# Kernel tuning notes

Hardware: AMD Instinct MI355X
Metric: run time of the kernel (lower is better)

Reference implementation:

```python
import jax, jax.numpy as jnp
import numpy as np

H = 1024      # hidden_size
E = 8         # num_experts
I = 1024      # moe_intermediate_size
SI = 2816     # shared_expert_intermediate_size
B, S = 2, 2048


def setup_inputs() -> dict:
    key = jax.random.key(0)
    ks = jax.random.split(key, 10)
    sc = lambda fan_in: 1.0 / np.sqrt(fan_in)
    return {
        "hidden_states": jax.random.normal(ks[0], (B, S, H), dtype=jnp.float32),
        "gate_w": jax.random.normal(ks[1], (E, H), dtype=jnp.float32) * sc(H),
        "wg": jax.random.normal(ks[2], (E, I, H), dtype=jnp.float32) * sc(H),   # gate_proj per expert
        "wu": jax.random.normal(ks[3], (E, I, H), dtype=jnp.float32) * sc(H),   # up_proj per expert
        "wd": jax.random.normal(ks[4], (E, H, I), dtype=jnp.float32) * sc(I),   # down_proj per expert
        "swg": jax.random.normal(ks[5], (SI, H), dtype=jnp.float32) * sc(H),    # shared gate_proj
        "swu": jax.random.normal(ks[6], (SI, H), dtype=jnp.float32) * sc(H),    # shared up_proj
        "swd": jax.random.normal(ks[7], (H, SI), dtype=jnp.float32) * sc(SI),   # shared down_proj
        "shared_gate_w": jax.random.normal(ks[8], (1, H), dtype=jnp.float32) * sc(H),
        "top_k": 2,
    }


def reference(hidden_states, gate_w, wg, wu, wd, swg, swu, swd, shared_gate_w, top_k):
    b, s, h = hidden_states.shape
    flat = hidden_states.reshape(-1, h)                      # [T,H]
    # router
    logits = flat @ gate_w.T                                 # [T,E]
    probs = jax.nn.softmax(logits, axis=-1)
    vals, idx = jax.lax.top_k(probs, top_k)                  # [T,K]
    vals = vals / jnp.sum(vals, axis=-1, keepdims=True)      # norm_topk_prob
    # combine weights scattered to full expert dim: [T,E]
    combine = jnp.sum(jax.nn.one_hot(idx, E, dtype=flat.dtype) * vals[..., None], axis=1)
    # dense per-expert SwiGLU FFN over all tokens, masked-combined (same math)
    g = jax.nn.silu(jnp.einsum("th,eih->eti", flat, wg))     # [E,T,I]
    u = jnp.einsum("th,eih->eti", flat, wu)
    eo = jnp.einsum("eti,ehi->eth", g * u, wd)               # [E,T,H]
    expert_out = jnp.einsum("te,eth->th", combine, eo)       # [T,H]
    # shared expert with sigmoid gate
    shared = (jax.nn.silu(flat @ swg.T) * (flat @ swu.T)) @ swd.T   # [T,H]
    sgate = jax.nn.sigmoid(flat @ shared_gate_w.T)           # [T,1]
    out = expert_out + sgate * shared
    return out.reshape(b, s, h)
```

## Files before the change

kernel.cpp:

```cpp
#include <hip/hip_runtime.h>
#include <stdint.h>

#define TT  4096
#define HD  1024
#define NE  8
#define ID  1024
#define SID 2816

typedef short s16x8 __attribute__((ext_vector_type(8)));
typedef float f32x4 __attribute__((ext_vector_type(4)));
typedef float f32x4v __attribute__((ext_vector_type(4)));
typedef unsigned short u16x4 __attribute__((ext_vector_type(4)));

__device__ __forceinline__ ushort f2bf(float f) {
  uint32_t u = __float_as_uint(f);
  u += 0x7FFFu + ((u >> 16) & 1u);
  return (ushort)(u >> 16);
}

__device__ __forceinline__ float bf2f(ushort u) {
  return __uint_as_float((uint32_t)u << 16);
}

__device__ __forceinline__ void gll16(const ushort* g, ushort* l) {
  __builtin_amdgcn_global_load_lds(
      (const __attribute__((address_space(1))) void*)g,
      (__attribute__((address_space(3))) void*)l, 16, 0, 0);
}

struct CvtArgs {
  const float* src[7];
  ushort* dst[7];
  int n[7];
};

__global__ __launch_bounds__(256) void cvt_all(CvtArgs a) {
  int t = blockIdx.y;
  int i = (blockIdx.x * 256 + threadIdx.x) * 4;
  if (i >= a.n[t]) return;
  f32x4v v = *(const f32x4v*)(a.src[t] + i);
  u16x4 o;
  o.x = f2bf(v.x); o.y = f2bf(v.y); o.z = f2bf(v.z); o.w = f2bf(v.w);
  *(u16x4*)(a.dst[t] + i) = o;
}

__global__ __launch_bounds__(256) void router_k(
    const float* __restrict__ X, const float* __restrict__ gw,
    const float* __restrict__ sgw,
    int* __restrict__ topki, float* __restrict__ topkw,
    float* __restrict__ sgate) {
  __shared__ float gwL[(NE + 1) * HD];
  #pragma unroll
  for (int i = 0; i < NE * HD / 1024; i++) {
    int idx = i * 1024 + threadIdx.x * 4;
    *(f32x4*)&gwL[idx] = *(const f32x4*)&gw[idx];
  }
  {
    int idx = threadIdx.x * 4;
    if (idx < HD) *(f32x4*)&gwL[NE * HD + idx] = *(const f32x4*)&sgw[idx];
  }
  __syncthreads();

  const int wave = threadIdx.x >> 6, lane = threadIdx.x & 63;
  #pragma unroll
  for (int tt = 0; tt < 4; tt++) {
    const int t = blockIdx.x * 16 + wave * 4 + tt;
    const float* x = X + (size_t)t * HD;
    float acc[NE + 1];
    #pragma unroll
    for (int e = 0; e <= NE; e++) acc[e] = 0.f;
    #pragma unroll
    for (int p = 0; p < HD / 256; p++) {
      const int k = p * 256 + lane * 4;
      f32x4 xv = *(const f32x4*)&x[k];
      #pragma unroll
      for (int e = 0; e < NE; e++) {
        f32x4 g = *(const f32x4*)&gwL[e * HD + k];
        acc[e] += xv.x * g.x + xv.y * g.y + xv.z * g.z + xv.w * g.w;
      }
      f32x4 s = *(const f32x4*)&gwL[NE * HD + k];
      acc[NE] += xv.x * s.x + xv.y * s.y + xv.z * s.z + xv.w * s.w;
    }
    #pragma unroll
    for (int off = 32; off > 0; off >>= 1)
      #pragma unroll
      for (int e = 0; e <= NE; e++)
        acc[e] += __shfl_xor(acc[e], off, 64);
    if (lane == 0) {
      float m = acc[0];
      #pragma unroll
      for (int e = 1; e < NE; e++) m = fmaxf(m, acc[e]);
      float p[NE];
      #pragma unroll
      for (int e = 0; e < NE; e++) p[e] = __expf(acc[e] - m);
      int i1 = 0;
      #pragma unroll
      for (int e = 1; e < NE; e++) if (p[e] > p[i1]) i1 = e;
      int i2 = (i1 == 0) ? 1 : 0;
      #pragma unroll
      for (int e = 0; e < NE; e++) if (e != i1 && p[e] > p[i2]) i2 = e;
      float inv = 1.f / (p[i1] + p[i2]);
      topki[2 * t] = i1; topki[2 * t + 1] = i2;
      topkw[2 * t] = p[i1] * inv; topkw[2 * t + 1] = p[i2] * inv;
      sgate[t] = 1.f / (1.f + __expf(-acc[NE]));
    }
  }
}

__global__ __launch_bounds__(1024) void binning_k(
    const int* __restrict__ topki, const float* __restrict__ topkw,
    int* __restrict__ cnt, int* __restrict__ offs,
    int* __restrict__ tokmap, float* __restrict__ wmap,
    int* __restrict__ smap) {
  __shared__ int h[NE];
  __shared__ int base[NE];
  const int tid = threadIdx.x;
  if (tid < NE) h[tid] = 0;
  __syncthreads();
  int my_e[8];
  #pragma unroll
  for (int i = 0; i < 8; i++) {
    int s = i * 1024 + tid;
    my_e[i] = topki[s];
    atomicAdd(&h[my_e[i]], 1);
  }
  __syncthreads();
  if (tid == 0) {
    int o = 0;
    for (int e = 0; e < NE; e++) {
      base[e] = o; offs[e] = o; cnt[e] = h[e]; o += h[e];
    }
  }
  __syncthreads();
  #pragma unroll
  for (int i = 0; i < 8; i++) {
    int s = i * 1024 + tid;
    int pos = atomicAdd(&base[my_e[i]], 1);
    tokmap[pos] = s >> 1;
    wmap[pos] = topkw[s];
    smap[s] = pos;
  }
}

constexpr int BM = 128, BN = 128, BK = 32;

template <bool GATHER>
__device__ __forceinline__ void gu_core(
    const ushort* __restrict__ A, const ushort* __restrict__ Wg,
    const ushort* __restrict__ Wu, ushort* __restrict__ Hout,
    const int* __restrict__ tokmap, int cnt, int seg,
    int mb, int nb, int N, int K) {
  const int m0 = mb * BM;
  if (m0 >= cnt) return;
  const int n0 = nb * BN;

  __shared__ ushort lA[2][BM * BK];
  __shared__ ushort lBg[2][BN * BK];
  __shared__ ushort lBu[2][BN * BK];

  const int tid = threadIdx.x;
  const int wave = tid >> 6, lane = tid & 63;
  const int wm = (wave >> 1) * 64, wn = (wave & 1) * 64;

  const int ar0 = wave * 32 + (lane >> 2);
  const int ar1 = ar0 + 16;
  const int kc = ((lane & 3) ^ ((lane >> 3) & 3)) * 8;

  const ushort *a0p, *a1p;
  if (GATHER) {
    int m_ = m0 + ar0;
    int tk0 = (m_ < cnt) ? tokmap[seg + m_] : 0;
    m_ = m0 + ar1;
    int tk1 = (m_ < cnt) ? tokmap[seg + m_] : 0;
    a0p = A + (size_t)tk0 * K + kc;
    a1p = A + (size_t)tk1 * K + kc;
  } else {
    a0p = A + (size_t)(m0 + ar0) * K + kc;
    a1p = A + (size_t)(m0 + ar1) * K + kc;
  }
  const ushort* bg0 = Wg + (size_t)(n0 + ar0) * K + kc;
  const ushort* bg1 = Wg + (size_t)(n0 + ar1) * K + kc;
  const ushort* bu0 = Wu + (size_t)(n0 + ar0) * K + kc;
  const ushort* bu1 = Wu + (size_t)(n0 + ar1) * K + kc;

  f32x4 accG[4][4], accU[4][4];
  #pragma unroll
  for (int i = 0; i < 4; i++)
    #pragma unroll
    for (int j = 0; j < 4; j++) {
      accG[i][j] = f32x4{0.f, 0.f, 0.f, 0.f};
      accU[i][j] = f32x4{0.f, 0.f, 0.f, 0.f};
    }

  const int lr = lane & 15;
  const int lk = (((lane >> 4) ^ ((lr >> 1) & 3))) * 8;
  const int w32 = wave * 32;

  auto stage = [&](int b, int k0) {
    gll16(a0p + k0, &lA[b][w32 * BK]);
    gll16(a1p + k0, &lA[b][(w32 + 16) * BK]);
    gll16(bg0 + k0, &lBg[b][w32 * BK]);
    gll16(bg1 + k0, &lBg[b][(w32 + 16) * BK]);
    gll16(bu0 + k0, &lBu[b][w32 * BK]);
    gll16(bu1 + k0, &lBu[b][(w32 + 16) * BK]);
  };

  const int nt = K / BK;
  stage(0, 0);
  for (int t = 0; t < nt; t++) {
    const int cur = t & 1;
    if (t + 1 < nt) {
      stage(cur ^ 1, (t + 1) * BK);
      asm volatile("s_waitcnt vmcnt(6)" ::: "memory");
    } else {
      asm volatile("s_waitcnt vmcnt(0)" ::: "memory");
    }
    __builtin_amdgcn_s_barrier();

    s16x8 af[4], bgf[4], buf_[4];
    #pragma unroll
    for (int i = 0; i < 4; i++) {
      af[i]   = *(const s16x8*)&lA [cur][(wm + i * 16 + lr) * BK + lk];
      bgf[i]  = *(const s16x8*)&lBg[cur][(wn + i * 16 + lr) * BK + lk];
      buf_[i] = *(const s16x8*)&lBu[cur][(wn + i * 16 + lr) * BK + lk];
    }
    #pragma unroll
    for (int i = 0; i < 4; i++)
      #pragma unroll
      for (int j = 0; j < 4; j++) {
        accG[i][j] = __builtin_amdgcn_mfma_f32_16x16x32_bf16(af[i], bgf[j], accG[i][j], 0, 0, 0);
        accU[i][j] = __builtin_amdgcn_mfma_f32_16x16x32_bf16(af[i], buf_[j], accU[i][j], 0, 0, 0);
      }
    __builtin_amdgcn_s_barrier();
  }

  const int lrr = (lane >> 4) * 4;
  #pragma unroll
  for (int i = 0; i < 4; i++) {
    #pragma unroll
    for (int r = 0; r < 4; r++) {
      int m = wm + i * 16 + lrr + r;
      if (m0 + m < cnt) {
        size_t row = (size_t)(seg + m0 + m) * N;
        #pragma unroll
        for (int j = 0; j < 4; j++) {
          int c = n0 + wn + j * 16 + lr;
          float g = accG[i][j][r];
          float u = accU[i][j][r];
          float s = g / (1.f + __expf(-g));
          Hout[row + c] = f2bf(s * u);
        }
      }
    }
  }
}

template <bool GATHER>
__device__ __forceinline__ void dn_core(
    const ushort* __restrict__ A, const ushort* __restrict__ W,
    ushort* __restrict__ outB, float* __restrict__ outF,
    const float* __restrict__ sgate, int cnt, int seg,
    int mb, int nb, int N, int K) {
  const int m0 = mb * BM;
  if (m0 >= cnt) return;
  const int n0 = nb * BN;

  __shared__ ushort lA[2][BM * BK];
  __shared__ ushort lB[2][BN * BK];

  const int tid = threadIdx.x;
  const int wave = tid >> 6, lane = tid & 63;
  const int wm = (wave >> 1) * 64, wn = (wave & 1) * 64;

  const int ar0 = wave * 32 + (lane >> 2);
  const int ar1 = ar0 + 16;
  const int kc = ((lane & 3) ^ ((lane >> 3) & 3)) * 8;

  int r0 = m0 + ar0; if (r0 > cnt - 1) r0 = cnt - 1;
  int r1 = m0 + ar1; if (r1 > cnt - 1) r1 = cnt - 1;
  const ushort* a0p = A + (size_t)(seg + r0) * K + kc;
  const ushort* a1p = A + (size_t)(seg + r1) * K + kc;
  const ushort* b0 = W + (size_t)(n0 + ar0) * K + kc;
  const ushort* b1 = W + (size_t)(n0 + ar1) * K + kc;

  f32x4 acc[4][4];
  #pragma unroll
  for (int i = 0; i < 4; i++)
    #pragma unroll
    for (int j = 0; j < 4; j++) acc[i][j] = f32x4{0.f, 0.f, 0.f, 0.f};

  const int lr = lane & 15;
  const int lk = (((lane >> 4) ^ ((lr >> 1) & 3))) * 8;
  const int w32 = wave * 32;

  auto stage = [&](int b, int k0) {
    gll16(a0p + k0, &lA[b][w32 * BK]);
    gll16(a1p + k0, &lA[b][(w32 + 16) * BK]);
    gll16(b0 + k0, &lB[b][w32 * BK]);
    gll16(b1 + k0, &lB[b][(w32 + 16) * BK]);
  };

  const int nt = K / BK;
  stage(0, 0);
  for (int t = 0; t < nt; t++) {
    const int cur = t & 1;
    if (t + 1 < nt) {
      stage(cur ^ 1, (t + 1) * BK);
      asm volatile("s_waitcnt vmcnt(4)" ::: "memory");
    } else {
      asm volatile("s_waitcnt vmcnt(0)" ::: "memory");
    }
    __builtin_amdgcn_s_barrier();

    s16x8 af[4], bf[4];
    #pragma unroll
    for (int i = 0; i < 4; i++) {
      af[i] = *(const s16x8*)&lA[cur][(wm + i * 16 + lr) * BK + lk];
      bf[i] = *(const s16x8*)&lB[cur][(wn + i * 16 + lr) * BK + lk];
    }
    #pragma unroll
    for (int i = 0; i < 4; i++)
      #pragma unroll
      for (int j = 0; j < 4; j++)
        acc[i][j] = __builtin_amdgcn_mfma_f32_16x16x32_bf16(af[i], bf[j], acc[i][j], 0, 0, 0);
    __builtin_amdgcn_s_barrier();
  }

  const int lrr = (lane >> 4) * 4;
  #pragma unroll
  for (int i = 0; i < 4; i++) {
    #pragma unroll
    for (int r = 0; r < 4; r++) {
      int m = wm + i * 16 + lrr + r;
      if (m0 + m < cnt) {
        if (GATHER) {
          size_t row = (size_t)(seg + m0 + m) * N;
          #pragma unroll
          for (int j = 0; j < 4; j++) {
            int c = n0 + wn + j * 16 + lr;
            outB[row + c] = f2bf(acc[i][j][r]);
          }
        } else {
          int t = m0 + m;
          float wv = sgate[t];
          size_t row = (size_t)t * N;
          #pragma unroll
          for (int j = 0; j < 4; j++) {
            int c = n0 + wn + j * 16 + lr;
            outF[row + c] = wv * acc[i][j][r];
          }
        }
      }
    }
  }
}

__global__ __launch_bounds__(256, 2) void gemm_gu_s(
    const ushort* __restrict__ A, const ushort* __restrict__ Wg,
    const ushort* __restrict__ Wu, ushort* __restrict__ H,
    int M, int N, int K) {
  int id = blockIdx.x;
  int x = id & 7, k = id >> 3;
  int mb = (x & 3) * 8 + (k & 7);
  int nb = (x >> 2) * 11 + (k >> 3);
  gu_core<false>(A, Wg, Wu, H, nullptr, M, 0, mb, nb, N, K);
}

__global__ __launch_bounds__(256, 2) void gemm_gu_r(
    const ushort* __restrict__ A, const ushort* __restrict__ Wg,
    const ushort* __restrict__ Wu, ushort* __restrict__ H,
    const int* __restrict__ tokmap, const int* __restrict__ cnts,
    const int* __restrict__ offs, int N, int K) {
  int e = blockIdx.x;
  gu_core<true>(A, Wg + (size_t)e * N * K, Wu + (size_t)e * N * K, H,
                tokmap, cnts[e], offs[e], blockIdx.y, blockIdx.z, N, K);
}

__global__ __launch_bounds__(256, 2) void gemm_dn_s(
    const ushort* __restrict__ A, const ushort* __restrict__ W,
    float* __restrict__ out, const float* __restrict__ sgate,
    int M, int N, int K) {
  int id = blockIdx.x;
  int x = id & 7, k = id >> 3;
  int mb = x * 4 + (k & 3);
  int nb = k >> 2;
  dn_core<false>(A, W, nullptr, out, sgate, M, 0, mb, nb, N, K);
}

__global__ __launch_bounds__(256, 2) void gemm_dn_r(
    const ushort* __restrict__ A, const ushort* __restrict__ W,
    ushort* __restrict__ eo, const int* __restrict__ cnts,
    const int* __restrict__ offs, int N, int K) {
  int e = blockIdx.x;
  dn_core<true>(A, W + (size_t)e * N * K, eo, nullptr, nullptr,
                cnts[e], offs[e], blockIdx.y, blockIdx.z, N, K);
}

__global__ __launch_bounds__(256) void combine_k(
    const ushort* __restrict__ eo, const float* __restrict__ topkw,
    const int* __restrict__ smap, float* __restrict__ out) {
  int t = blockIdx.x;
  int c = threadIdx.x * 4;
  int s0 = smap[2 * t], s1 = smap[2 * t + 1];
  float w0 = topkw[2 * t], w1 = topkw[2 * t + 1];
  u16x4 a = *(const u16x4*)&eo[(size_t)s0 * HD + c];
  u16x4 b = *(const u16x4*)&eo[(size_t)s1 * HD + c];
  float* o = out + (size_t)t * HD + c;
  f32x4 ov = *(const f32x4*)o;
  #pragma unroll
  for (int j = 0; j < 4; j++)
    ov[j] += w0 * bf2f(a[j]) + w1 * bf2f(b[j]);
  *(f32x4*)o = ov;
}

extern "C" void kernel_launch(void* const* d_in, const int* in_sizes, int n_in,
                              void* d_out, int out_size, void* d_ws, size_t ws_size,
                              hipStream_t stream) {
  const float* hs  = (const float*)d_in[0];
  const float* gw  = (const float*)d_in[1];
  const float* wg  = (const float*)d_in[2];
  const float* wu  = (const float*)d_in[3];
  const float* wd  = (const float*)d_in[4];
  const float* swg = (const float*)d_in[5];
  const float* swu = (const float*)d_in[6];
  const float* swd = (const float*)d_in[7];
  const float* sgw = (const float*)d_in[8];
  float* out = (float*)d_out;

  uint8_t* base = (uint8_t*)d_ws;
  size_t off = 0;
  auto give = [&](size_t b) -> void* {
    void* p = base + off;
    off += (b + 255) & ~(size_t)255;
    return p;
  };
  ushort* Xb   = (ushort*)give((size_t)TT * HD * 2);
  ushort* wgB  = (ushort*)give((size_t)NE * ID * HD * 2);
  ushort* wuB  = (ushort*)give((size_t)NE * ID * HD * 2);
  ushort* wdB  = (ushort*)give((size_t)NE * HD * ID * 2);
  ushort* sgB  = (ushort*)give((size_t)SID * HD * 2);
  ushort* suB  = (ushort*)give((size_t)SID * HD * 2);
  ushort* sdB  = (ushort*)give((size_t)HD * SID * 2);
  ushort* Sbuf = (ushort*)give((size_t)TT * SID * 2);
  ushort* Hbuf = (ushort*)give((size_t)2 * TT * ID * 2);
  float* sgate = (float*)give(TT * 4);
  int* topki   = (int*)give(TT * 2 * 4);
  float* topkw = (float*)give(TT * 2 * 4);
  int* tokmap  = (int*)give(2 * TT * 4);
  float* wmap  = (float*)give(2 * TT * 4);
  int* smap    = (int*)give(2 * TT * 4);
  int* cnt     = (int*)give(256);
  int* offs    = (int*)give(256);

  CvtArgs ca;
  ca.src[0] = hs;  ca.dst[0] = Xb;  ca.n[0] = TT * HD;
  ca.src[1] = wg;  ca.dst[1] = wgB; ca.n[1] = NE * ID * HD;
  ca.src[2] = wu;  ca.dst[2] = wuB; ca.n[2] = NE * ID * HD;
  ca.src[3] = wd;  ca.dst[3] = wdB; ca.n[3] = NE * HD * ID;
  ca.src[4] = swg; ca.dst[4] = sgB; ca.n[4] = SID * HD;
  ca.src[5] = swu; ca.dst[5] = suB; ca.n[5] = SID * HD;
  ca.src[6] = swd; ca.dst[6] = sdB; ca.n[6] = HD * SID;
  cvt_all<<<dim3(8192, 7), 256, 0, stream>>>(ca);

  router_k<<<TT / 16, 256, 0, stream>>>(hs, gw, sgw, topki, topkw, sgate);
  binning_k<<<1, 1024, 0, stream>>>(topki, topkw, cnt, offs, tokmap, wmap, smap);

  gemm_gu_s<<<(TT / BM) * (SID / BN), 256, 0, stream>>>(
      Xb, sgB, suB, Sbuf, TT, SID, HD);
  gemm_dn_s<<<(TT / BM) * (HD / BN), 256, 0, stream>>>(
      Sbuf, sdB, out, sgate, TT, HD, SID);

  gemm_gu_r<<<dim3(NE, 2 * TT / BM, ID / BN), 256, 0, stream>>>(
      Xb, wgB, wuB, Hbuf, tokmap, cnt, offs, ID, HD);
  gemm_dn_r<<<dim3(NE, 2 * TT / BM, HD / BN), 256, 0, stream>>>(
      Hbuf, wdB, Sbuf , cnt, offs, HD, ID);

  combine_k<<<TT, 256, 0, stream>>>(Sbuf, topkw, smap, out);
}
```

Baseline: 288.5 us.

## Fuse hidden-state bf16 conversion into router, widen cvt, retile shared down GEMM

The fp32-to-bf16 conversion of the hidden states moves into the router kernel, which already reads them, so that pass over the activations is no longer a separate read. The weight conversion kernel now handles 16 elements per thread on a smaller grid. The shared-expert down projection becomes its own kernel with 128x64 tiles instead of 128x128, doubling the block count to about 512 to improve occupancy and load balance across CUs, at the cost of more A-tile reloads.

Result: slower. 305.4 us (+5.9%).

```diff
diff --git a/kernel.cpp b/kernel.cpp
--- a/kernel.cpp
+++ b/kernel.cpp
@@ -29,24 +29,29 @@
 }
 
 struct CvtArgs {
-  const float* src[7];
-  ushort* dst[7];
-  int n[7];
+  const float* src[6];
+  ushort* dst[6];
+  int n[6];
 };
 
 __global__ __launch_bounds__(256) void cvt_all(CvtArgs a) {
   int t = blockIdx.y;
-  int i = (blockIdx.x * 256 + threadIdx.x) * 4;
-  if (i >= a.n[t]) return;
-  f32x4v v = *(const f32x4v*)(a.src[t] + i);
-  u16x4 o;
-  o.x = f2bf(v.x); o.y = f2bf(v.y); o.z = f2bf(v.z); o.w = f2bf(v.w);
-  *(u16x4*)(a.dst[t] + i) = o;
+  int base = (blockIdx.x * 256 + threadIdx.x) * 16;
+  if (base >= a.n[t]) return;
+  const float* s = a.src[t] + base;
+  ushort* d = a.dst[t] + base;
+  #pragma unroll
+  for (int j = 0; j < 4; j++) {
+    f32x4v v = *(const f32x4v*)(s + j * 4);
+    u16x4 o;
+    o.x = f2bf(v.x); o.y = f2bf(v.y); o.z = f2bf(v.z); o.w = f2bf(v.w);
+    *(u16x4*)(d + j * 4) = o;
+  }
 }
 
 __global__ __launch_bounds__(256) void router_k(
     const float* __restrict__ X, const float* __restrict__ gw,
-    const float* __restrict__ sgw,
+    const float* __restrict__ sgw, ushort* __restrict__ Xb,
     int* __restrict__ topki, float* __restrict__ topkw,
     float* __restrict__ sgate) {
   __shared__ float gwL[(NE + 1) * HD];
@@ -73,6 +78,9 @@
     for (int p = 0; p < HD / 256; p++) {
       const int k = p * 256 + lane * 4;
       f32x4 xv = *(const f32x4*)&x[k];
+      u16x4 xb;
+      xb.x = f2bf(xv.x); xb.y = f2bf(xv.y); xb.z = f2bf(xv.z); xb.w = f2bf(xv.w);
+      *(u16x4*)&Xb[(size_t)t * HD + k] = xb;
       #pragma unroll
       for (int e = 0; e < NE; e++) {
         f32x4 g = *(const f32x4*)&gwL[e * HD + k];
@@ -255,11 +263,9 @@
   }
 }
 
-template <bool GATHER>
 __device__ __forceinline__ void dn_core(
     const ushort* __restrict__ A, const ushort* __restrict__ W,
-    ushort* __restrict__ outB, float* __restrict__ outF,
-    const float* __restrict__ sgate, int cnt, int seg,
+    ushort* __restrict__ outB, int cnt, int seg,
     int mb, int nb, int N, int K) {
   const int m0 = mb * BM;
   if (m0 >= cnt) return;
@@ -333,22 +339,11 @@
     for (int r = 0; r < 4; r++) {
       int m = wm + i * 16 + lrr + r;
       if (m0 + m < cnt) {
-        if (GATHER) {
-          size_t row = (size_t)(seg + m0 + m) * N;
-          #pragma unroll
-          for (int j = 0; j < 4; j++) {
-            int c = n0 + wn + j * 16 + lr;
-            outB[row + c] = f2bf(acc[i][j][r]);
-          }
-        } else {
-          int t = m0 + m;
-          float wv = sgate[t];
-          size_t row = (size_t)t * N;
-          #pragma unroll
-          for (int j = 0; j < 4; j++) {
-            int c = n0 + wn + j * 16 + lr;
-            outF[row + c] = wv * acc[i][j][r];
-          }
+        size_t row = (size_t)(seg + m0 + m) * N;
+        #pragma unroll
+        for (int j = 0; j < 4; j++) {
+          int c = n0 + wn + j * 16 + lr;
+          outB[row + c] = f2bf(acc[i][j][r]);
         }
       }
     }
@@ -381,10 +376,85 @@
     float* __restrict__ out, const float* __restrict__ sgate,
     int M, int N, int K) {
   int id = blockIdx.x;
-  int x = id & 7, k = id >> 3;
-  int mb = x * 4 + (k & 3);
-  int nb = k >> 2;
-  dn_core<false>(A, W, nullptr, out, sgate, M, 0, mb, nb, N, K);
+  int x = id & 7, kk = id >> 3;
+  int mb = x * 4 + (kk & 3);
+  int nb = kk >> 2;
+  const int m0 = mb * 128, n0 = nb * 64;
+
+  __shared__ ushort lA[2][128 * 32];
+  __shared__ ushort lB[2][64 * 32];
+
+  const int tid = threadIdx.x;
+  const int wave = tid >> 6, lane = tid & 63;
+  const int wm = (wave >> 1) * 64, wn = (wave & 1) * 32;
+
+  const int ar0 = wave * 32 + (lane >> 2);
+  const int ar1 = ar0 + 16;
+  const int br  = wave * 16 + (lane >> 2);
+  const int kc = ((lane & 3) ^ ((lane >> 3) & 3)) * 8;
+
+  const ushort* a0p = A + (size_t)(m0 + ar0) * K + kc;
+  const ushort* a1p = A + (size_t)(m0 + ar1) * K + kc;
+  const ushort* bp  = W + (size_t)(n0 + br) * K + kc;
+
+  f32x4 acc[4][2];
+  #pragma unroll
+  for (int i = 0; i < 4; i++)
+    #pragma unroll
+    for (int j = 0; j < 2; j++) acc[i][j] = f32x4{0.f, 0.f, 0.f, 0.f};
+
+  const int lr = lane & 15;
+  const int lk = (((lane >> 4) ^ ((lr >> 1) & 3))) * 8;
+  const int w32 = wave * 32;
+
+  auto stage = [&](int b, int k0) {
+    gll16(a0p + k0, &lA[b][w32 * 32]);
+    gll16(a1p + k0, &lA[b][(w32 + 16) * 32]);
+    gll16(bp + k0, &lB[b][wave * 512]);
+  };
+
+  const int nt = K / 32;
+  stage(0, 0);
+  for (int t = 0; t < nt; t++) {
+    const int cur = t & 1;
+    if (t + 1 < nt) {
+      stage(cur ^ 1, (t + 1) * 32);
+      asm volatile("s_waitcnt vmcnt(3)" ::: "memory");
+    } else {
+      asm volatile("s_waitcnt vmcnt(0)" ::: "memory");
+    }
+    __builtin_amdgcn_s_barrier();
+
+    s16x8 af[4], bf[2];
+    #pragma unroll
+    for (int i = 0; i < 4; i++)
+      af[i] = *(const s16x8*)&lA[cur][(wm + i * 16 + lr) * 32 + lk];
+    #pragma unroll
+    for (int j = 0; j < 2; j++)
+      bf[j] = *(const s16x8*)&lB[cur][(wn + j * 16 + lr) * 32 + lk];
+    #pragma unroll
+    for (int i = 0; i < 4; i++)
+      #pragma unroll
+      for (int j = 0; j < 2; j++)
+        acc[i][j] = __builtin_amdgcn_mfma_f32_16x16x32_bf16(af[i], bf[j], acc[i][j], 0, 0, 0);
+    __builtin_amdgcn_s_barrier();
+  }
+
+  const int lrr = (lane >> 4) * 4;
+  #pragma unroll
+  for (int i = 0; i < 4; i++) {
+    #pragma unroll
+    for (int r = 0; r < 4; r++) {
+      int m = m0 + wm + i * 16 + lrr + r;
+      float wv = sgate[m];
+      size_t row = (size_t)m * N;
+      #pragma unroll
+      for (int j = 0; j < 2; j++) {
+        int c = n0 + wn + j * 16 + lr;
+        out[row + c] = wv * acc[i][j][r];
+      }
+    }
+  }
 }
 
 __global__ __launch_bounds__(256, 2) void gemm_dn_r(
@@ -392,8 +462,8 @@
     ushort* __restrict__ eo, const int* __restrict__ cnts,
     const int* __restrict__ offs, int N, int K) {
   int e = blockIdx.x;
-  dn_core<true>(A, W + (size_t)e * N * K, eo, nullptr, nullptr,
-                cnts[e], offs[e], blockIdx.y, blockIdx.z, N, K);
+  dn_core(A, W + (size_t)e * N * K, eo, cnts[e], offs[e],
+          blockIdx.y, blockIdx.z, N, K);
 }
 
 __global__ __launch_bounds__(256) void combine_k(
@@ -453,21 +523,20 @@
   int* offs    = (int*)give(256);
 
   CvtArgs ca;
-  ca.src[0] = hs;  ca.dst[0] = Xb;  ca.n[0] = TT * HD;
-  ca.src[1] = wg;  ca.dst[1] = wgB; ca.n[1] = NE * ID * HD;
-  ca.src[2] = wu;  ca.dst[2] = wuB; ca.n[2] = NE * ID * HD;
-  ca.src[3] = wd;  ca.dst[3] = wdB; ca.n[3] = NE * HD * ID;
-  ca.src[4] = swg; ca.dst[4] = sgB; ca.n[4] = SID * HD;
-  ca.src[5] = swu; ca.dst[5] = suB; ca.n[5] = SID * HD;
-  ca.src[6] = swd; ca.dst[6] = sdB; ca.n[6] = HD * SID;
-  cvt_all<<<dim3(8192, 7), 256, 0, stream>>>(ca);
-
-  router_k<<<TT / 16, 256, 0, stream>>>(hs, gw, sgw, topki, topkw, sgate);
+  ca.src[0] = wg;  ca.dst[0] = wgB; ca.n[0] = NE * ID * HD;
+  ca.src[1] = wu;  ca.dst[1] = wuB; ca.n[1] = NE * ID * HD;
+  ca.src[2] = wd;  ca.dst[2] = wdB; ca.n[2] = NE * HD * ID;
+  ca.src[3] = swg; ca.dst[3] = sgB; ca.n[3] = SID * HD;
+  ca.src[4] = swu; ca.dst[4] = suB; ca.n[4] = SID * HD;
+  ca.src[5] = swd; ca.dst[5] = sdB; ca.n[5] = HD * SID;
+  cvt_all<<<dim3(2048, 6), 256, 0, stream>>>(ca);
+
+  router_k<<<TT / 16, 256, 0, stream>>>(hs, gw, sgw, Xb, topki, topkw, sgate);
   binning_k<<<1, 1024, 0, stream>>>(topki, topkw, cnt, offs, tokmap, wmap, smap);
 
   gemm_gu_s<<<(TT / BM) * (SID / BN), 256, 0, stream>>>(
       Xb, sgB, suB, Sbuf, TT, SID, HD);
-  gemm_dn_s<<<(TT / BM) * (HD / BN), 256, 0, stream>>>(
+  gemm_dn_s<<<(TT / 128) * (HD / 64), 256, 0, stream>>>(
       Sbuf, sdB, out, sgate, TT, HD, SID);
 
   gemm_gu_r<<<dim3(NE, 2 * TT / BM, ID / BN), 256, 0, stream>>>(
```
